# Kernel tuning notes

Measured on AMD Instinct MI355X. Metric: run time of the kernel, lower is better.

## Reference

```python
import jax, jax.numpy as jnp
import numpy as np

EPS = 1e-4
GRID_RES = 0.01
L = 2
ATOL = 0.01
RTOL = 1e-5


def compute_lub(f_v, edges):
    # f_v: [V,2] vertex filtration values; edges: [E,2] int vertex indices
    e_x = jnp.max(f_v[:, 0][edges], axis=1)  # [E]
    e_y = jnp.max(f_v[:, 1][edges], axis=1)  # [E]
    f_e = jnp.stack([e_x, e_y], axis=1) + EPS  # [E,2]
    return jnp.concatenate([f_v, f_e], axis=0)  # [V+E, 2] = [S,2]


def grad_matrices(filtration, bar, sample_pts):
    # filtration: [S,2], bar: [P,R], sample_pts: [P,2]
    # Vectorized version of the per-point Python loops in moveSimplices.forward.
    S = filtration.shape[0]
    P = sample_pts.shape[0]
    fx, fy = filtration[:, 0], filtration[:, 1]          # [S]
    px, py = sample_pts[:, 0], sample_pts[:, 1]          # [P]
    fsum = fx + fy                                        # [S]
    psum = px + py                                        # [P]
    shift = jnp.arange(-L, L + 1, dtype=filtration.dtype)  # [5]
    tol_x = ATOL + RTOL * jnp.abs(fx)                     # torch.isclose tolerance
    tol_y = ATOL + RTOL * jnp.abs(fy)
    below = fsum[None, :] < psum[:, None]                 # [P,S]
    above = fsum[None, :] > psum[:, None]

    Gs, Gcs = [], []
    for r in range(bar.shape[1]):  # small fixed rank loop (R=3)
        s = bar[:, r] + GRID_RES                          # [P]
        line_x = shift[None, :] * s[:, None] + px[:, None]  # [P,5]
        line_y = shift[None, :] * s[:, None] + py[:, None]
        last_x, last_y = line_x[:, -1], line_y[:, -1]      # [P] (shift=+L endpoint)
        # isclose over shifts, reduced with any() (duplicate scatter writes are idempotent)
        hit_x = (jnp.abs(line_x[:, None, :] - fx[None, :, None]) <= tol_x[None, :, None]).any(-1)  # [P,S]
        hit_y = (jnp.abs(line_y[:, None, :] - fy[None, :, None]) <= tol_y[None, :, None]).any(-1)
        lx = hit_x & (fy[None, :] <= last_y[:, None]) & below
        ux = hit_x & (fy[None, :] <= last_y[:, None]) & above
        ly = hit_y & (fx[None, :] <= last_x[:, None]) & below
        uy = hit_y & (fx[None, :] <= last_x[:, None]) & above
        vx = ux.astype(filtration.dtype) - lx.astype(filtration.dtype)  # +1 upper, -1 lower (exclusive)
        vy = uy.astype(filtration.dtype) - ly.astype(filtration.dtype)
        G = jnp.stack([vx, vy], axis=-1).reshape(P, 2 * S)  # interleave x,y columns
        cx = jnp.where(ux.any(1), -1.0, jnp.where(lx.any(1), 1.0, 0.0)).astype(filtration.dtype)
        cy = jnp.where(uy.any(1), -1.0, jnp.where(ly.any(1), 1.0, 0.0)).astype(filtration.dtype)
        Gc = jnp.stack([cx, cy], axis=-1)                  # [P,2]
        Gs.append(G)
        Gcs.append(Gc)
    return jnp.stack(Gs), jnp.stack(Gcs)  # [R,P,2S], [R,P,2]


def setup_inputs() -> dict:
    key = jax.random.key(0)
    k1, k2, k3, k4, k5 = jax.random.split(key, 5)
    V, E, P, R = 1200, 4800, 2500, 3
    f_v = jax.random.uniform(k1, (V, 2), dtype=jnp.float32)
    edges = jax.random.randint(k2, (E, 2), 0, V, dtype=jnp.int64)
    bars0 = jax.random.uniform(k3, (P, R), dtype=jnp.float32)
    bars1 = jax.random.uniform(k4, (P, R), dtype=jnp.float32)
    sample_pts = jax.random.uniform(k5, (P, 2), dtype=jnp.float32)
    return {"f_v": f_v, "edges": edges, "bars0": bars0, "bars1": bars1, "sample_pts": sample_pts}


def reference(f_v, edges, bars0, bars1, sample_pts):
    filtration = compute_lub(f_v, edges)
    G0, Gc0 = grad_matrices(filtration, bars0, sample_pts)
    G1, Gc1 = grad_matrices(filtration, bars1, sample_pts)
    # moveSimplices.forward returns the bars unchanged; the grad matrices are the
    # saved side outputs (ctx.grad_matrices_*) and the kernel-heavy computation.
    return (bars0, bars1, G0, G1, Gc0, Gc1)
```

## Files before the change

### kernel.cpp

```cpp
#include <hip/hip_runtime.h>

#define EPS_F      1e-4f
#define GRID_RES_F 0.01f
#define ATOL_F     0.01f
#define RTOL_F     1e-5f

static constexpr int V = 1200;
static constexpr int E = 4800;
static constexpr int S = V + E;
static constexpr int P = 2500;
static constexpr int R = 3;

static constexpr size_t G0_BASE  = 15000ull;
static constexpr size_t ROW_LEN  = 2ull * S;
static constexpr size_t G_ELEMS  = (size_t)R * P * ROW_LEN;
static constexpr size_t GC0_BASE = G0_BASE + 2 * G_ELEMS;

__global__ void build_filt_kernel(const float* __restrict__ f_v,
                                  const int*   __restrict__ edges,
                                  float4*      __restrict__ filt) {
    int j = blockIdx.x * blockDim.x + threadIdx.x;
    if (j >= S) return;
    float fx, fy;
    if (j < V) {
        fx = f_v[2 * j];
        fy = f_v[2 * j + 1];
    } else {
        int e = j - V;
        int a = edges[2 * e];
        int b = edges[2 * e + 1];
        fx = __fadd_rn(fmaxf(f_v[2 * a],     f_v[2 * b]),     EPS_F);
        fy = __fadd_rn(fmaxf(f_v[2 * a + 1], f_v[2 * b + 1]), EPS_F);
    }
    float tolx = __fadd_rn(ATOL_F, __fmul_rn(RTOL_F, fabsf(fx)));
    float toly = __fadd_rn(ATOL_F, __fmul_rn(RTOL_F, fabsf(fy)));
    filt[j] = make_float4(fx, fy, tolx, toly);
}

__device__ __forceinline__ float mindist(const float* l, float f) {
    float a = fabsf(__fsub_rn(l[0], f));
    float b = fabsf(__fsub_rn(l[1], f));
    float c = fabsf(__fsub_rn(l[2], f));
    float d = fabsf(__fsub_rn(l[3], f));
    float e = fabsf(__fsub_rn(l[4], f));
    return fminf(fminf(fminf(a, b), fminf(c, d)), e);
}

__device__ __forceinline__ void cell(const float4& f, float psum,
                                     const float* lxs, const float* lys,
                                     float& vx, float& vy,
                                     int& aux, int& alx, int& auy, int& aly) {
    float fsum = __fadd_rn(f.x, f.y);
    bool ab = fsum > psum, be = fsum < psum;
    float sg = ab ? 1.0f : (be ? -1.0f : 0.0f);
    bool cx = (mindist(lxs, f.x) <= f.z) && (f.y <= lys[4]);
    bool cy = (mindist(lys, f.y) <= f.w) && (f.x <= lxs[4]);
    vx = cx ? sg : 0.0f;
    vy = cy ? sg : 0.0f;
    aux |= (int)(cx && ab); alx |= (int)(cx && be);
    auy |= (int)(cy && ab); aly |= (int)(cy && be);
}

__global__ __launch_bounds__(256) void grad_kernel(
        const float4* __restrict__ filt,
        const float*  __restrict__ bars0,
        const float*  __restrict__ bars1,
        const float*  __restrict__ sample_pts,
        float*        __restrict__ d_out) {
    const int p = blockIdx.x;
    const int r = blockIdx.y;
    const int b = blockIdx.z;

    const float* bar = (b == 0) ? bars0 : bars1;
    const float px = sample_pts[2 * p];
    const float py = sample_pts[2 * p + 1];
    const float psum = __fadd_rn(px, py);
    const float s  = __fadd_rn(bar[p * R + r], GRID_RES_F);
    const float s2 = __fmul_rn(2.0f, s);

    float lxs[5], lys[5];
    lxs[0] = __fadd_rn(-s2, px); lxs[1] = __fadd_rn(-s, px); lxs[2] = px;
    lxs[3] = __fadd_rn( s, px);  lxs[4] = __fadd_rn(s2, px);
    lys[0] = __fadd_rn(-s2, py); lys[1] = __fadd_rn(-s, py); lys[2] = py;
    lys[3] = __fadd_rn( s, py);  lys[4] = __fadd_rn(s2, py);

    float* Grow = d_out + G0_BASE + (size_t)b * G_ELEMS
                        + ((size_t)(r * P + p)) * ROW_LEN;

    __shared__ int shw[4][4];
    const int lane = threadIdx.x & 63;
    const int wv   = threadIdx.x >> 6;

    int aux = 0, alx = 0, auy = 0, aly = 0;

    int c0 = wv * 256 + 2 * lane;
    int c1 = c0 + 128;
    float4 a0 = {}, a1 = {}, a2 = {}, a3 = {};
    if (c0 < S) { a0 = filt[c0]; a1 = filt[c0 + 1]; }
    if (c1 < S) { a2 = filt[c1]; a3 = filt[c1 + 1]; }
    while (c0 < S) {
        const int c0n = c0 + 1024, c1n = c1 + 1024;
        float4 b0 = {}, b1 = {}, b2 = {}, b3 = {};
        if (c0n < S) { b0 = filt[c0n]; b1 = filt[c0n + 1]; }
        if (c1n < S) { b2 = filt[c1n]; b3 = filt[c1n + 1]; }

        {
            float4 o;
            cell(a0, psum, lxs, lys, o.x, o.y, aux, alx, auy, aly);
            cell(a1, psum, lxs, lys, o.z, o.w, aux, alx, auy, aly);
            *reinterpret_cast<float4*>(Grow + 2 * (size_t)c0) = o;
        }
        if (c1 < S) {
            float4 o;
            cell(a2, psum, lxs, lys, o.x, o.y, aux, alx, auy, aly);
            cell(a3, psum, lxs, lys, o.z, o.w, aux, alx, auy, aly);
            *reinterpret_cast<float4*>(Grow + 2 * (size_t)c1) = o;
        }
        a0 = b0; a1 = b1; a2 = b2; a3 = b3;
        c0 = c0n; c1 = c1n;
    }

    int f0 = __any(aux), f1 = __any(alx), f2 = __any(auy), f3 = __any(aly);
    if (lane == 0) {
        shw[wv][0] = f0; shw[wv][1] = f1; shw[wv][2] = f2; shw[wv][3] = f3;
    }
    __syncthreads();
    if (threadIdx.x == 0) {
        int ux = shw[0][0] | shw[1][0] | shw[2][0] | shw[3][0];
        int lx = shw[0][1] | shw[1][1] | shw[2][1] | shw[3][1];
        int uy = shw[0][2] | shw[1][2] | shw[2][2] | shw[3][2];
        int ly = shw[0][3] | shw[1][3] | shw[2][3] | shw[3][3];
        float cx = ux ? -1.0f : (lx ? 1.0f : 0.0f);
        float cy = uy ? -1.0f : (ly ? 1.0f : 0.0f);
        size_t gc = GC0_BASE + (size_t)b * ((size_t)R * P * 2)
                             + ((size_t)(r * P + p)) * 2;
        d_out[gc]     = cx;
        d_out[gc + 1] = cy;
    }
}

extern "C" void kernel_launch(void* const* d_in, const int* in_sizes, int n_in,
                              void* d_out, int out_size, void* d_ws, size_t ws_size,
                              hipStream_t stream) {
    const float* f_v        = (const float*)d_in[0];
    const int*   edges      = (const int*)d_in[1];
    const float* bars0      = (const float*)d_in[2];
    const float* bars1      = (const float*)d_in[3];
    const float* sample_pts = (const float*)d_in[4];
    float* out = (float*)d_out;

    float4* filt = (float4*)d_ws;

    (void)hipMemcpyAsync(out,         bars0, (size_t)P * R * sizeof(float),
                         hipMemcpyDeviceToDevice, stream);
    (void)hipMemcpyAsync(out + P * R, bars1, (size_t)P * R * sizeof(float),
                         hipMemcpyDeviceToDevice, stream);

    build_filt_kernel<<<(S + 255) / 256, 256, 0, stream>>>(f_v, edges, filt);

    grad_kernel<<<dim3(P, R, 2), 256, 0, stream>>>(filt, bars0, bars1,
                                                   sample_pts, out);
}
```

Measured before the change: 734.4 us.

## Flatten grad kernel into grid-stride loop with atomic flag reduction

Replaces the one-block-per-row grid (15000 blocks of 256 threads) with a persistent grid-stride kernel over all float4 output chunks. Each thread computes two cells and writes one float4. The per-row any-reductions move to wave-level votes and atomicOr into a flags buffer, which a new small kernel turns into the Gc outputs. This removes per-block setup, the shared-memory barrier and tail imbalance, at the cost of per-element index divisions, recomputing the line points per element, atomics, and an extra launch.

```diff
diff --git a/kernel.cpp b/kernel.cpp
--- a/kernel.cpp
+++ b/kernel.cpp
@@ -11,6 +11,12 @@
 static constexpr int P = 2500;
 static constexpr int R = 3;
 
+static constexpr int NROWS      = 2 * R * P;
+static constexpr int F4_PER_ROW = 3000;
+static constexpr unsigned Q4    = (unsigned)NROWS * F4_PER_ROW;
+
+static constexpr int NBLK = 2048, BS = 256;
+
 static constexpr size_t G0_BASE  = 15000ull;
 static constexpr size_t ROW_LEN  = 2ull * S;
 static constexpr size_t G_ELEMS  = (size_t)R * P * ROW_LEN;
@@ -18,8 +24,10 @@
 
 __global__ void build_filt_kernel(const float* __restrict__ f_v,
                                   const int*   __restrict__ edges,
-                                  float4*      __restrict__ filt) {
+                                  float4*      __restrict__ filt,
+                                  int*         __restrict__ flags) {
     int j = blockIdx.x * blockDim.x + threadIdx.x;
+    if (j < NROWS) flags[j] = 0;
     if (j >= S) return;
     float fx, fy;
     if (j < V) {
@@ -66,77 +74,67 @@
         const float*  __restrict__ bars0,
         const float*  __restrict__ bars1,
         const float*  __restrict__ sample_pts,
-        float*        __restrict__ d_out) {
-    const int p = blockIdx.x;
-    const int r = blockIdx.y;
-    const int b = blockIdx.z;
+        float*        __restrict__ d_out,
+        int*          __restrict__ flags) {
+    const unsigned stride = (unsigned)NBLK * BS;
+    for (unsigned q = blockIdx.x * (unsigned)BS + threadIdx.x; q < Q4;
+         q += stride) {
+        const unsigned rid = q / (unsigned)F4_PER_ROW;
+        const unsigned w   = q - rid * (unsigned)F4_PER_ROW;
+        const unsigned b   = rid / (unsigned)(R * P);
+        const unsigned rem = rid - b * (unsigned)(R * P);
+        const unsigned r   = rem / (unsigned)P;
+        const unsigned p   = rem - r * (unsigned)P;
 
-    const float* bar = (b == 0) ? bars0 : bars1;
-    const float px = sample_pts[2 * p];
-    const float py = sample_pts[2 * p + 1];
-    const float psum = __fadd_rn(px, py);
-    const float s  = __fadd_rn(bar[p * R + r], GRID_RES_F);
-    const float s2 = __fmul_rn(2.0f, s);
+        const float* bar = b ? bars1 : bars0;
+        const float px = sample_pts[2 * p];
+        const float py = sample_pts[2 * p + 1];
+        const float psum = __fadd_rn(px, py);
+        const float s  = __fadd_rn(bar[p * R + r], GRID_RES_F);
+        const float s2 = __fmul_rn(2.0f, s);
 
-    float lxs[5], lys[5];
-    lxs[0] = __fadd_rn(-s2, px); lxs[1] = __fadd_rn(-s, px); lxs[2] = px;
-    lxs[3] = __fadd_rn( s, px);  lxs[4] = __fadd_rn(s2, px);
-    lys[0] = __fadd_rn(-s2, py); lys[1] = __fadd_rn(-s, py); lys[2] = py;
-    lys[3] = __fadd_rn( s, py);  lys[4] = __fadd_rn(s2, py);
+        float lxs[5], lys[5];
+        lxs[0] = __fadd_rn(-s2, px); lxs[1] = __fadd_rn(-s, px); lxs[2] = px;
+        lxs[3] = __fadd_rn( s, px);  lxs[4] = __fadd_rn(s2, px);
+        lys[0] = __fadd_rn(-s2, py); lys[1] = __fadd_rn(-s, py); lys[2] = py;
+        lys[3] = __fadd_rn( s, py);  lys[4] = __fadd_rn(s2, py);
 
-    float* Grow = d_out + G0_BASE + (size_t)b * G_ELEMS
-                        + ((size_t)(r * P + p)) * ROW_LEN;
+        const unsigned j = 2 * w;
+        const float4 a0 = filt[j];
+        const float4 a1 = filt[j + 1];
 
-    __shared__ int shw[4][4];
-    const int lane = threadIdx.x & 63;
-    const int wv   = threadIdx.x >> 6;
+        int aux = 0, alx = 0, auy = 0, aly = 0;
+        float4 o;
+        cell(a0, psum, lxs, lys, o.x, o.y, aux, alx, auy, aly);
+        cell(a1, psum, lxs, lys, o.z, o.w, aux, alx, auy, aly);
+        *reinterpret_cast<float4*>(d_out + G0_BASE + 4 * (size_t)q) = o;
 
-    int aux = 0, alx = 0, auy = 0, aly = 0;
+        int bits = aux | (alx << 1) | (auy << 2) | (aly << 3);
+        if (__any(bits)) {
+            const unsigned rid0 = (unsigned)__shfl((int)rid, 0);
+            if (__all(rid == rid0)) {
+                int f0 = __any(aux) ? 1 : 0;
+                int f1 = __any(alx) ? 1 : 0;
+                int f2 = __any(auy) ? 1 : 0;
+                int f3 = __any(aly) ? 1 : 0;
+                if ((threadIdx.x & 63) == 0)
+                    atomicOr(&flags[rid0], f0 | (f1 << 1) | (f2 << 2) | (f3 << 3));
+            } else if (bits) {
+                atomicOr(&flags[rid], bits);
+            }
+        }
+    }
+}
 
-    int c0 = wv * 256 + 2 * lane;
-    int c1 = c0 + 128;
-    float4 a0 = {}, a1 = {}, a2 = {}, a3 = {};
-    if (c0 < S) { a0 = filt[c0]; a1 = filt[c0 + 1]; }
-    if (c1 < S) { a2 = filt[c1]; a3 = filt[c1 + 1]; }
-    while (c0 < S) {
-        const int c0n = c0 + 1024, c1n = c1 + 1024;
-        float4 b0 = {}, b1 = {}, b2 = {}, b3 = {};
-        if (c0n < S) { b0 = filt[c0n]; b1 = filt[c0n + 1]; }
-        if (c1n < S) { b2 = filt[c1n]; b3 = filt[c1n + 1]; }
-
-        {
-            float4 o;
-            cell(a0, psum, lxs, lys, o.x, o.y, aux, alx, auy, aly);
-            cell(a1, psum, lxs, lys, o.z, o.w, aux, alx, auy, aly);
-            *reinterpret_cast<float4*>(Grow + 2 * (size_t)c0) = o;
-        }
-        if (c1 < S) {
-            float4 o;
-            cell(a2, psum, lxs, lys, o.x, o.y, aux, alx, auy, aly);
-            cell(a3, psum, lxs, lys, o.z, o.w, aux, alx, auy, aly);
-            *reinterpret_cast<float4*>(Grow + 2 * (size_t)c1) = o;
-        }
-        a0 = b0; a1 = b1; a2 = b2; a3 = b3;
-        c0 = c0n; c1 = c1n;
-    }
-
-    int f0 = __any(aux), f1 = __any(alx), f2 = __any(auy), f3 = __any(aly);
-    if (lane == 0) {
-        shw[wv][0] = f0; shw[wv][1] = f1; shw[wv][2] = f2; shw[wv][3] = f3;
-    }
-    __syncthreads();
-    if (threadIdx.x == 0) {
-        int ux = shw[0][0] | shw[1][0] | shw[2][0] | shw[3][0];
-        int lx = shw[0][1] | shw[1][1] | shw[2][1] | shw[3][1];
-        int uy = shw[0][2] | shw[1][2] | shw[2][2] | shw[3][2];
-        int ly = shw[0][3] | shw[1][3] | shw[2][3] | shw[3][3];
-        float cx = ux ? -1.0f : (lx ? 1.0f : 0.0f);
-        float cy = uy ? -1.0f : (ly ? 1.0f : 0.0f);
-        size_t gc = GC0_BASE + (size_t)b * ((size_t)R * P * 2)
-                             + ((size_t)(r * P + p)) * 2;
-        d_out[gc]     = cx;
-        d_out[gc + 1] = cy;
-    }
+__global__ void gc_kernel(const int* __restrict__ flags,
+                          float* __restrict__ d_out) {
+    int rid = blockIdx.x * blockDim.x + threadIdx.x;
+    if (rid >= NROWS) return;
+    int f = flags[rid];
+    float cx = (f & 1) ? -1.0f : ((f & 2) ? 1.0f : 0.0f);
+    float cy = (f & 4) ? -1.0f : ((f & 8) ? 1.0f : 0.0f);
+    d_out[GC0_BASE + 2 * (size_t)rid]     = cx;
+    d_out[GC0_BASE + 2 * (size_t)rid + 1] = cy;
 }
 
 extern "C" void kernel_launch(void* const* d_in, const int* in_sizes, int n_in,
@@ -149,15 +147,19 @@
     const float* sample_pts = (const float*)d_in[4];
     float* out = (float*)d_out;
 
-    float4* filt = (float4*)d_ws;
+    float4* filt  = (float4*)d_ws;
+    int*    flags = (int*)d_ws + S * 4;
 
     (void)hipMemcpyAsync(out,         bars0, (size_t)P * R * sizeof(float),
                          hipMemcpyDeviceToDevice, stream);
     (void)hipMemcpyAsync(out + P * R, bars1, (size_t)P * R * sizeof(float),
                          hipMemcpyDeviceToDevice, stream);
 
-    build_filt_kernel<<<(S + 255) / 256, 256, 0, stream>>>(f_v, edges, filt);
+    build_filt_kernel<<<(NROWS + 255) / 256, 256, 0, stream>>>(f_v, edges,
+                                                               filt, flags);
 
-    grad_kernel<<<dim3(P, R, 2), 256, 0, stream>>>(filt, bars0, bars1,
-                                                   sample_pts, out);
+    grad_kernel<<<dim3(NBLK), BS, 0, stream>>>(filt, bars0, bars1,
+                                               sample_pts, out, flags);
+
+    gc_kernel<<<(NROWS + 255) / 256, 256, 0, stream>>>(flags, out);
 }
```

After: 814.5 us. +10.9%, slower.
